# Optimization experiments

Hardware: AMD Instinct MI355X
Metric: run time of the kernel (lower is better)

## Reference

```python
import jax, jax.numpy as jnp
import numpy as np

B, S, D, M, E, K = 2, 2048, 1024, 1408, 8, 2  # batch, seq, n_embed, n_moe_mlp, n_experts, top_k


def setup_inputs() -> dict:
    key = jax.random.key(0)
    k0, k1, k2, k3, k4 = jax.random.split(key, 5)
    scale = 0.02
    return {
        "x": jax.random.normal(k0, (B, S, D), dtype=jnp.float32),
        "w_gate": jax.random.normal(k1, (D, E), dtype=jnp.float32) * scale,  # gate.weight.T
        "w_g": jax.random.normal(k2, (E, D, M), dtype=jnp.float32) * scale,  # gate_proj.weight.T per expert
        "w_u": jax.random.normal(k3, (E, D, M), dtype=jnp.float32) * scale,  # up_proj.weight.T per expert
        "w_d": jax.random.normal(k4, (E, M, D), dtype=jnp.float32) * scale,  # down_proj.weight.T per expert
    }


def reference(x, w_gate, w_g, w_u, w_d):
    # router
    scores = x @ w_gate                                  # [B,S,E]
    topk_scores, topk_idx = jax.lax.top_k(scores, K)     # [B,S,K]
    topk_probs = jax.nn.softmax(topk_scores, axis=-1)    # softmax over selected experts only
    # scatter top-k probs back to dense [B,S,E] gating (top_k indices are distinct)
    gating = jnp.sum(
        jax.nn.one_hot(topk_idx, E, dtype=topk_probs.dtype) * topk_probs[..., None],
        axis=-2,
    )                                                    # [B,S,E]
    # dense all-expert SwiGLU (faithful to the compute-then-mask original)
    hidden = jax.nn.silu(jnp.einsum("bsd,edm->ebsm", x, w_g)) * jnp.einsum(
        "bsd,edm->ebsm", x, w_u
    )                                                    # [E,B,S,M]
    expert_out = jnp.einsum("ebsm,emd->ebsd", hidden, w_d)  # [E,B,S,D]
    # masked weighted combine
    y = jnp.einsum("bse,ebsd->bsd", gating, expert_out)  # [B,S,D]
    return y
```

## Files before the change

kernel.cpp:

```cpp
#include <hip/hip_runtime.h>
#include <cstdio>

constexpr int T  = 4096;
constexpr int D  = 1024;
constexpr int M  = 1408;
constexpr int E  = 8;

constexpr int TM = 128;
constexpr int TN = 128;
constexpr int BK = 32;
constexpr int RCAP = T * 2 + E * TM;
constexpr int MT_MAX = T / TM;
constexpr int NT_UP = M / TN;
constexpr int NT_DN = D / TN;

constexpr int CSTR = 64;
constexpr int TOKB = 64;

typedef _Float16 half8 __attribute__((ext_vector_type(8)));
typedef _Float16 half4 __attribute__((ext_vector_type(4)));
typedef float    floatx4 __attribute__((ext_vector_type(4)));

constexpr size_t OFF_COUNTS = 0;
constexpr size_t OFF_BASE   = (size_t)E * CSTR * 4;
constexpr size_t OFF_PC     = OFF_BASE + 64;
constexpr size_t OFF_TOTAL  = OFF_PC + 64;
constexpr size_t OFF_T2E    = OFF_TOTAL + 64;
constexpr size_t OFF_T2POS  = OFF_T2E   + (size_t)2 * T * 4;
constexpr size_t OFF_T2P    = OFF_T2POS + (size_t)2 * T * 4;
constexpr size_t OFF_TLIST  = OFF_T2P   + (size_t)2 * T * 4;
constexpr size_t OFF_XG     = OFF_TLIST + (size_t)E * T * 4;
constexpr size_t OFF_HID    = OFF_XG  + (size_t)RCAP * D * 2;
constexpr size_t OFF_WGT    = OFF_HID + (size_t)RCAP * M * 2;
constexpr size_t OFF_WUT    = OFF_WGT + (size_t)E * M * D * 2;
constexpr size_t OFF_WDT    = OFF_WUT + (size_t)E * M * D * 2;
constexpr size_t WS_NEED    = OFF_WDT + (size_t)E * D * M * 2;

__device__ __forceinline__ void gl_lds16(const void* g, void* l) {
  __builtin_amdgcn_global_load_lds(
      (const __attribute__((address_space(1))) unsigned int*)g,
      (__attribute__((address_space(3))) unsigned int*)l, 16, 0, 0);
}

__global__ __launch_bounds__(256) void k_router(
    const float* __restrict__ x, const float* __restrict__ wgate,
    int* __restrict__ counts, int* __restrict__ tlist,
    int* __restrict__ t2e, int* __restrict__ t2pos, float* __restrict__ t2p) {
  __shared__ int   s_cnt[E];
  __shared__ int   s_base[E];
  __shared__ int   s_e[2 * TOKB];
  __shared__ int   s_pos[2 * TOKB];
  __shared__ float s_p[2 * TOKB];
  int wv = threadIdx.x >> 6, lane = threadIdx.x & 63;
  if (threadIdx.x < E) s_cnt[threadIdx.x] = 0;
  __syncthreads();

  for (int j = 0; j < TOKB / 4; ++j) {
    int tl = wv * (TOKB / 4) + j;
    int t  = blockIdx.x * TOKB + tl;
    const float* xr = x + (size_t)t * D;
    float acc[E] = {0.f,0.f,0.f,0.f,0.f,0.f,0.f,0.f};
    #pragma unroll
    for (int i = 0; i < D / 64; ++i) {
      int d = i * 64 + lane;
      float xv = xr[d];
      const float4* wr2 = (const float4*)(wgate + (size_t)d * E);
      float4 w0 = wr2[0], w1 = wr2[1];
      acc[0] += xv * w0.x; acc[1] += xv * w0.y; acc[2] += xv * w0.z; acc[3] += xv * w0.w;
      acc[4] += xv * w1.x; acc[5] += xv * w1.y; acc[6] += xv * w1.z; acc[7] += xv * w1.w;
    }
    #pragma unroll
    for (int e = 0; e < E; ++e) {
      #pragma unroll
      for (int off = 32; off; off >>= 1) acc[e] += __shfl_xor(acc[e], off, 64);
    }
    if (lane == 0) {
      int i0 = 0; float s0 = acc[0];
      #pragma unroll
      for (int e = 1; e < E; ++e) if (acc[e] > s0) { s0 = acc[e]; i0 = e; }
      int i1 = -1; float s1 = -1e30f;
      #pragma unroll
      for (int e = 0; e < E; ++e) if (e != i0 && acc[e] > s1) { s1 = acc[e]; i1 = e; }
      float p0 = 1.f / (1.f + expf(s1 - s0));
      float p1 = 1.f - p0;
      int q0 = atomicAdd(&s_cnt[i0], 1);
      int q1 = atomicAdd(&s_cnt[i1], 1);
      s_e[2 * tl]     = i0; s_pos[2 * tl]     = q0; s_p[2 * tl]     = p0;
      s_e[2 * tl + 1] = i1; s_pos[2 * tl + 1] = q1; s_p[2 * tl + 1] = p1;
    }
  }
  __syncthreads();
  if (threadIdx.x < E)
    s_base[threadIdx.x] = atomicAdd(&counts[threadIdx.x * CSTR], s_cnt[threadIdx.x]);
  __syncthreads();
  if (threadIdx.x < 2 * TOKB) {
    int sl = threadIdx.x;
    int e = s_e[sl];
    int pos = s_base[e] + s_pos[sl];
    int t = blockIdx.x * TOKB + (sl >> 1);
    tlist[e * T + pos] = t;
    t2e[2 * t + (sl & 1)]   = e;
    t2pos[2 * t + (sl & 1)] = pos;
    t2p[2 * t + (sl & 1)]   = s_p[sl];
  }
}

__global__ void k_scan(const int* __restrict__ counts, int* __restrict__ base,
                       int* __restrict__ pc, int* __restrict__ total) {
  if (threadIdx.x == 0 && blockIdx.x == 0) {
    int b = 0;
    for (int e = 0; e < E; ++e) {
      base[e] = b;
      int p = (counts[e * CSTR] + TM - 1) / TM * TM;
      pc[e] = p; b += p;
    }
    *total = b;
  }
}

__global__ __launch_bounds__(256) void k_gather(
    const float* __restrict__ x, const int* __restrict__ counts,
    const int* __restrict__ base, const int* __restrict__ pc,
    const int* __restrict__ total, const int* __restrict__ tlist,
    _Float16* __restrict__ Xg) {
  int r = blockIdx.x;
  if (r >= *total) return;
  int e = 0;
  while (e < E - 1 && r >= base[e] + pc[e]) ++e;
  int local = r - base[e];
  int d = threadIdx.x * 4;
  union { _Float16 h[4]; ushort4 u; } o;
  if (local < counts[e * CSTR]) {
    int t = tlist[e * T + local];
    float4 v = *(const float4*)(x + (size_t)t * D + d);
    o.h[0] = (_Float16)v.x; o.h[1] = (_Float16)v.y;
    o.h[2] = (_Float16)v.z; o.h[3] = (_Float16)v.w;
  } else {
    o.h[0] = (_Float16)0.f; o.h[1] = (_Float16)0.f;
    o.h[2] = (_Float16)0.f; o.h[3] = (_Float16)0.f;
  }
  *(ushort4*)(Xg + (size_t)r * D + d) = o.u;
}

__global__ __launch_bounds__(256) void k_transpose(
    const float* __restrict__ src, _Float16* __restrict__ dst, int R, int C) {
  __shared__ float tile[32][33];
  int e = blockIdx.z, rt = blockIdx.y, ct = blockIdx.x;
  int tr  = threadIdx.x >> 3;
  int tc4 = (threadIdx.x & 7) * 4;
  const float* s = src + ((size_t)e * R + rt * 32 + tr) * C + ct * 32 + tc4;
  float4 v = *(const float4*)s;
  tile[tr][tc4 + 0] = v.x; tile[tr][tc4 + 1] = v.y;
  tile[tr][tc4 + 2] = v.z; tile[tr][tc4 + 3] = v.w;
  __syncthreads();
  union { _Float16 h[4]; ushort4 u; } o;
  #pragma unroll
  for (int i = 0; i < 4; ++i) o.h[i] = (_Float16)tile[tc4 + i][tr];
  *(ushort4*)(dst + ((size_t)e * C + ct * 32 + tr) * R + rt * 32 + tc4) = o.u;
}

__global__ __launch_bounds__(256, 2) void k_upgate(
    const _Float16* __restrict__ Xg, const _Float16* __restrict__ wgT,
    const _Float16* __restrict__ wuT, _Float16* __restrict__ Hid,
    const int* __restrict__ base, const int* __restrict__ pc) {
  int lin = blockIdx.x;
  int e = lin & 7;
  int r = lin >> 3;
  int nt = r % NT_UP;
  int mt = r / NT_UP;
  if (mt * TM >= pc[e]) return;
  int row0 = base[e] + mt * TM;
  int n0 = nt * TN;
  __shared__ _Float16 As[TM * BK];
  __shared__ _Float16 Bg[TN * BK];
  __shared__ _Float16 Bu[TN * BK];
  int tid = threadIdx.x;
  int w = tid >> 6, lane = tid & 63;
  int lrow = lane & 15, quad = lane >> 4;
  int wr = w >> 1, wc = w & 1;
  int sr = lane >> 2, sc = (lane & 3) * 8;

  const _Float16* wg_e = wgT + (size_t)e * M * D;
  const _Float16* wu_e = wuT + (size_t)e * M * D;
  const _Float16* pA0 = Xg + (size_t)(row0 + w * 32 + sr) * D + sc;
  const _Float16* pA1 = Xg + (size_t)(row0 + w * 32 + 16 + sr) * D + sc;
  const _Float16* pG0 = wg_e + (size_t)(n0 + w * 32 + sr) * D + sc;
  const _Float16* pG1 = wg_e + (size_t)(n0 + w * 32 + 16 + sr) * D + sc;
  const _Float16* pU0 = wu_e + (size_t)(n0 + w * 32 + sr) * D + sc;
  const _Float16* pU1 = wu_e + (size_t)(n0 + w * 32 + 16 + sr) * D + sc;
  char* lA0 = (char*)As + (w * 2 + 0) * 1024;
  char* lA1 = (char*)As + (w * 2 + 1) * 1024;
  char* lG0 = (char*)Bg + (w * 2 + 0) * 1024;
  char* lG1 = (char*)Bg + (w * 2 + 1) * 1024;
  char* lU0 = (char*)Bu + (w * 2 + 0) * 1024;
  char* lU1 = (char*)Bu + (w * 2 + 1) * 1024;

  floatx4 accg[4][4] = {};
  floatx4 accu[4][4] = {};

  for (int k0 = 0; k0 < D; k0 += BK) {
    gl_lds16(pA0, lA0); gl_lds16(pA1, lA1);
    gl_lds16(pG0, lG0); gl_lds16(pG1, lG1);
    gl_lds16(pU0, lU0); gl_lds16(pU1, lU1);
    pA0 += BK; pA1 += BK; pG0 += BK; pG1 += BK; pU0 += BK; pU1 += BK;
    __syncthreads();
    half8 af[4];
    #pragma unroll
    for (int i = 0; i < 4; ++i)
      af[i] = *(const half8*)&As[(wr * 64 + i * 16 + lrow) * BK + quad * 8];
    #pragma unroll
    for (int c = 0; c < 4; ++c) {
      half8 bgc = *(const half8*)&Bg[(wc * 64 + c * 16 + lrow) * BK + quad * 8];
      half8 buc = *(const half8*)&Bu[(wc * 64 + c * 16 + lrow) * BK + quad * 8];
      #pragma unroll
      for (int i = 0; i < 4; ++i) {
        accg[c][i] = __builtin_amdgcn_mfma_f32_16x16x32_f16(af[i], bgc, accg[c][i], 0, 0, 0);
        accu[c][i] = __builtin_amdgcn_mfma_f32_16x16x32_f16(af[i], buc, accu[c][i], 0, 0, 0);
      }
    }
    __syncthreads();
  }
  #pragma unroll
  for (int c = 0; c < 4; ++c) {
    int col = n0 + wc * 64 + c * 16 + lrow;
    #pragma unroll
    for (int i = 0; i < 4; ++i) {
      int rowb = row0 + wr * 64 + i * 16 + quad * 4;
      #pragma unroll
      for (int reg = 0; reg < 4; ++reg) {
        float g = accg[c][i][reg], u = accu[c][i][reg];
        Hid[(size_t)(rowb + reg) * M + col] = (_Float16)(g / (1.f + expf(-g)) * u);
      }
    }
  }
}

__global__ __launch_bounds__(256, 2) void k_down(
    const _Float16* __restrict__ Hid, const _Float16* __restrict__ wdT,
    _Float16* __restrict__ Yp,
    const int* __restrict__ base, const int* __restrict__ pc) {
  int lin = blockIdx.x;
  int e = lin & 7;
  int r = lin >> 3;
  int nt = r % NT_DN;
  int mt = r / NT_DN;
  if (mt * TM >= pc[e]) return;
  int row0 = base[e] + mt * TM;
  int d0 = nt * TN;
  __shared__ _Float16 As[TM * BK];
  __shared__ _Float16 Bs[TN * BK];
  int tid = threadIdx.x;
  int w = tid >> 6, lane = tid & 63;
  int lrow = lane & 15, quad = lane >> 4;
  int wr = w >> 1, wc = w & 1;
  int sr = lane >> 2, sc = (lane & 3) * 8;

  const _Float16* wd_e = wdT + (size_t)e * D * M;
  const _Float16* pA0 = Hid + (size_t)(row0 + w * 32 + sr) * M + sc;
  const _Float16* pA1 = Hid + (size_t)(row0 + w * 32 + 16 + sr) * M + sc;
  const _Float16* pB0 = wd_e + (size_t)(d0 + w * 32 + sr) * M + sc;
  const _Float16* pB1 = wd_e + (size_t)(d0 + w * 32 + 16 + sr) * M + sc;
  char* lA0 = (char*)As + (w * 2 + 0) * 1024;
  char* lA1 = (char*)As + (w * 2 + 1) * 1024;
  char* lB0 = (char*)Bs + (w * 2 + 0) * 1024;
  char* lB1 = (char*)Bs + (w * 2 + 1) * 1024;

  floatx4 acc[4][4] = {};

  for (int k0 = 0; k0 < M; k0 += BK) {
    gl_lds16(pA0, lA0); gl_lds16(pA1, lA1);
    gl_lds16(pB0, lB0); gl_lds16(pB1, lB1);
    pA0 += BK; pA1 += BK; pB0 += BK; pB1 += BK;
    __syncthreads();
    half8 af[4];
    #pragma unroll
    for (int i = 0; i < 4; ++i)
      af[i] = *(const half8*)&As[(wr * 64 + i * 16 + lrow) * BK + quad * 8];
    #pragma unroll
    for (int c = 0; c < 4; ++c) {
      half8 bc = *(const half8*)&Bs[(wc * 64 + c * 16 + lrow) * BK + quad * 8];
      #pragma unroll
      for (int i = 0; i < 4; ++i)
        acc[c][i] = __builtin_amdgcn_mfma_f32_16x16x32_f16(af[i], bc, acc[c][i], 0, 0, 0);
    }
    __syncthreads();
  }
  #pragma unroll
  for (int c = 0; c < 4; ++c) {
    int col = d0 + wc * 64 + c * 16 + lrow;
    #pragma unroll
    for (int i = 0; i < 4; ++i) {
      int rowb = row0 + wr * 64 + i * 16 + quad * 4;
      #pragma unroll
      for (int reg = 0; reg < 4; ++reg)
        Yp[(size_t)(rowb + reg) * D + col] = (_Float16)acc[c][i][reg];
    }
  }
}

__global__ __launch_bounds__(256) void k_combine(
    const _Float16* __restrict__ Yp, const int* __restrict__ base,
    const int* __restrict__ t2e, const int* __restrict__ t2pos,
    const float* __restrict__ t2p, float* __restrict__ out) {
  int t = blockIdx.x;
  int r0 = base[t2e[2 * t]]     + t2pos[2 * t];
  int r1 = base[t2e[2 * t + 1]] + t2pos[2 * t + 1];
  float p0 = t2p[2 * t], p1 = t2p[2 * t + 1];
  int d = threadIdx.x * 4;
  half4 h0 = *(const half4*)(Yp + (size_t)r0 * D + d);
  half4 h1 = *(const half4*)(Yp + (size_t)r1 * D + d);
  float4 o;
  o.x = p0 * (float)h0.x + p1 * (float)h1.x;
  o.y = p0 * (float)h0.y + p1 * (float)h1.y;
  o.z = p0 * (float)h0.z + p1 * (float)h1.z;
  o.w = p0 * (float)h0.w + p1 * (float)h1.w;
  *(float4*)(out + (size_t)t * D + d) = o;
}

extern "C" void kernel_launch(void* const* d_in, const int* in_sizes, int n_in,
                              void* d_out, int out_size, void* d_ws, size_t ws_size,
                              hipStream_t stream) {
  const float* x     = (const float*)d_in[0];
  const float* wgate = (const float*)d_in[1];
  const float* w_g   = (const float*)d_in[2];
  const float* w_u   = (const float*)d_in[3];
  const float* w_d   = (const float*)d_in[4];
  float* out = (float*)d_out;
  char* ws = (char*)d_ws;

  if (ws_size < WS_NEED) {
    fprintf(stderr, "kernel_launch: ws_size=%zu < needed %zu\n", ws_size, WS_NEED);
    return;
  }

  int* counts = (int*)(ws + OFF_COUNTS);
  int* base   = (int*)(ws + OFF_BASE);
  int* pcn    = (int*)(ws + OFF_PC);
  int* total  = (int*)(ws + OFF_TOTAL);
  int* t2e    = (int*)(ws + OFF_T2E);
  int* t2pos  = (int*)(ws + OFF_T2POS);
  float* t2p  = (float*)(ws + OFF_T2P);
  int* tlist  = (int*)(ws + OFF_TLIST);
  _Float16* Xg  = (_Float16*)(ws + OFF_XG);
  _Float16* Hid = (_Float16*)(ws + OFF_HID);
  _Float16* wgT = (_Float16*)(ws + OFF_WGT);
  _Float16* wuT = (_Float16*)(ws + OFF_WUT);
  _Float16* wdT = (_Float16*)(ws + OFF_WDT);

  hipMemsetAsync(ws, 0, OFF_T2E, stream);

  k_router<<<T / TOKB, 256, 0, stream>>>(x, wgate, counts, tlist, t2e, t2pos, t2p);
  k_scan<<<1, 64, 0, stream>>>(counts, base, pcn, total);
  k_gather<<<RCAP, 256, 0, stream>>>(x, counts, base, pcn, total, tlist, Xg);

  k_transpose<<<dim3(M / 32, D / 32, E), 256, 0, stream>>>(w_g, wgT, D, M);
  k_transpose<<<dim3(M / 32, D / 32, E), 256, 0, stream>>>(w_u, wuT, D, M);
  k_transpose<<<dim3(D / 32, M / 32, E), 256, 0, stream>>>(w_d, wdT, M, D);

  k_upgate<<<E * MT_MAX * NT_UP, 256, 0, stream>>>(Xg, wgT, wuT, Hid, base, pcn);
  _Float16* Yp = Xg;
  k_down<<<E * MT_MAX * NT_DN, 256, 0, stream>>>(Hid, wdT, Yp, base, pcn);
  k_combine<<<T, 256, 0, stream>>>(Yp, base, t2e, t2pos, t2p, out);
}
```

Baseline: 348.6 us.

## Fuse router and weight transposes into one prep kernel, drop scan, double BK

Merges the router and the three weight transpose/cast kernels into a single k_prep launch, and shrinks the router token block so more blocks run. Removes the serial scan kernel by having each consumer recompute expert base offsets from the counts. Doubles the GEMM K-tile to 64 so each LDS stage feeds twice as many MFMAs per barrier, which doubles shared memory per block and may lower occupancy.

```diff
diff --git a/kernel.cpp b/kernel.cpp
--- a/kernel.cpp
+++ b/kernel.cpp
@@ -8,14 +8,17 @@
 
 constexpr int TM = 128;
 constexpr int TN = 128;
-constexpr int BK = 32;
+constexpr int BK = 64;
 constexpr int RCAP = T * 2 + E * TM;
 constexpr int MT_MAX = T / TM;
 constexpr int NT_UP = M / TN;
 constexpr int NT_DN = D / TN;
 
 constexpr int CSTR = 64;
-constexpr int TOKB = 64;
+constexpr int TOKB = 16;
+constexpr int RTB  = T / TOKB;
+constexpr int TP_PER_W = (M / 32) * (D / 32) * E;
+constexpr int PREP_GRID = RTB + 3 * TP_PER_W;
 
 typedef _Float16 half8 __attribute__((ext_vector_type(8)));
 typedef _Float16 half4 __attribute__((ext_vector_type(4)));
@@ -42,95 +45,128 @@
       (__attribute__((address_space(3))) unsigned int*)l, 16, 0, 0);
 }
 
-__global__ __launch_bounds__(256) void k_router(
+__device__ __forceinline__ void expert_base_pc(const int* __restrict__ counts,
+                                               int e, int& base_e, int& pc_e) {
+  int b = 0; base_e = 0; pc_e = 0;
+  #pragma unroll
+  for (int ee = 0; ee < E; ++ee) {
+    int c = counts[ee * CSTR];
+    int p = (c + TM - 1) / TM * TM;
+    if (ee == e) { base_e = b; pc_e = p; }
+    b += p;
+  }
+}
+
+__global__ __launch_bounds__(256) void k_prep(
     const float* __restrict__ x, const float* __restrict__ wgate,
+    const float* __restrict__ w_g, const float* __restrict__ w_u,
+    const float* __restrict__ w_d,
+    _Float16* __restrict__ wgT, _Float16* __restrict__ wuT, _Float16* __restrict__ wdT,
     int* __restrict__ counts, int* __restrict__ tlist,
     int* __restrict__ t2e, int* __restrict__ t2pos, float* __restrict__ t2p) {
+  __shared__ float tile[32][33];
   __shared__ int   s_cnt[E];
   __shared__ int   s_base[E];
   __shared__ int   s_e[2 * TOKB];
   __shared__ int   s_pos[2 * TOKB];
   __shared__ float s_p[2 * TOKB];
-  int wv = threadIdx.x >> 6, lane = threadIdx.x & 63;
-  if (threadIdx.x < E) s_cnt[threadIdx.x] = 0;
+  int bid = blockIdx.x;
+
+  if (bid < RTB) {
+    int wv = threadIdx.x >> 6, lane = threadIdx.x & 63;
+    if (threadIdx.x < E) s_cnt[threadIdx.x] = 0;
+    __syncthreads();
+    for (int j = 0; j < TOKB / 4; ++j) {
+      int tl = wv * (TOKB / 4) + j;
+      int t  = bid * TOKB + tl;
+      const float* xr = x + (size_t)t * D;
+      float acc[E] = {0.f,0.f,0.f,0.f,0.f,0.f,0.f,0.f};
+      #pragma unroll
+      for (int i = 0; i < D / 64; ++i) {
+        int d = i * 64 + lane;
+        float xv = xr[d];
+        const float4* wr2 = (const float4*)(wgate + (size_t)d * E);
+        float4 w0 = wr2[0], w1 = wr2[1];
+        acc[0] += xv * w0.x; acc[1] += xv * w0.y; acc[2] += xv * w0.z; acc[3] += xv * w0.w;
+        acc[4] += xv * w1.x; acc[5] += xv * w1.y; acc[6] += xv * w1.z; acc[7] += xv * w1.w;
+      }
+      #pragma unroll
+      for (int e = 0; e < E; ++e) {
+        #pragma unroll
+        for (int off = 32; off; off >>= 1) acc[e] += __shfl_xor(acc[e], off, 64);
+      }
+      if (lane == 0) {
+        int i0 = 0; float s0 = acc[0];
+        #pragma unroll
+        for (int e = 1; e < E; ++e) if (acc[e] > s0) { s0 = acc[e]; i0 = e; }
+        int i1 = -1; float s1 = -1e30f;
+        #pragma unroll
+        for (int e = 0; e < E; ++e) if (e != i0 && acc[e] > s1) { s1 = acc[e]; i1 = e; }
+        float p0 = 1.f / (1.f + expf(s1 - s0));
+        float p1 = 1.f - p0;
+        int q0 = atomicAdd(&s_cnt[i0], 1);
+        int q1 = atomicAdd(&s_cnt[i1], 1);
+        s_e[2 * tl]     = i0; s_pos[2 * tl]     = q0; s_p[2 * tl]     = p0;
+        s_e[2 * tl + 1] = i1; s_pos[2 * tl + 1] = q1; s_p[2 * tl + 1] = p1;
+      }
+    }
+    __syncthreads();
+    if (threadIdx.x < E)
+      s_base[threadIdx.x] = atomicAdd(&counts[threadIdx.x * CSTR], s_cnt[threadIdx.x]);
+    __syncthreads();
+    if (threadIdx.x < 2 * TOKB) {
+      int sl = threadIdx.x;
+      int e = s_e[sl];
+      int pos = s_base[e] + s_pos[sl];
+      int t = bid * TOKB + (sl >> 1);
+      tlist[e * T + pos] = t;
+      t2e[2 * t + (sl & 1)]   = e;
+      t2pos[2 * t + (sl & 1)] = pos;
+      t2p[2 * t + (sl & 1)]   = s_p[sl];
+    }
+    return;
+  }
+
+  int i = bid - RTB;
+  int which = i / TP_PER_W;
+  int j = i - which * TP_PER_W;
+  const float* src; _Float16* dst; int Rr, Cc;
+  if (which == 0)      { src = w_g; dst = wgT; Rr = D; Cc = M; }
+  else if (which == 1) { src = w_u; dst = wuT; Rr = D; Cc = M; }
+  else                 { src = w_d; dst = wdT; Rr = M; Cc = D; }
+  int ctn = Cc / 32, rtn = Rr / 32;
+  int e   = j / (ctn * rtn);
+  int rem = j - e * (ctn * rtn);
+  int rt = rem / ctn, ct = rem - rt * ctn;
+  int tr  = threadIdx.x >> 3;
+  int tc4 = (threadIdx.x & 7) * 4;
+  const float* s = src + ((size_t)e * Rr + rt * 32 + tr) * Cc + ct * 32 + tc4;
+  float4 v = *(const float4*)s;
+  tile[tr][tc4 + 0] = v.x; tile[tr][tc4 + 1] = v.y;
+  tile[tr][tc4 + 2] = v.z; tile[tr][tc4 + 3] = v.w;
   __syncthreads();
-
-  for (int j = 0; j < TOKB / 4; ++j) {
-    int tl = wv * (TOKB / 4) + j;
-    int t  = blockIdx.x * TOKB + tl;
-    const float* xr = x + (size_t)t * D;
-    float acc[E] = {0.f,0.f,0.f,0.f,0.f,0.f,0.f,0.f};
-    #pragma unroll
-    for (int i = 0; i < D / 64; ++i) {
-      int d = i * 64 + lane;
-      float xv = xr[d];
-      const float4* wr2 = (const float4*)(wgate + (size_t)d * E);
-      float4 w0 = wr2[0], w1 = wr2[1];
-      acc[0] += xv * w0.x; acc[1] += xv * w0.y; acc[2] += xv * w0.z; acc[3] += xv * w0.w;
-      acc[4] += xv * w1.x; acc[5] += xv * w1.y; acc[6] += xv * w1.z; acc[7] += xv * w1.w;
-    }
-    #pragma unroll
-    for (int e = 0; e < E; ++e) {
-      #pragma unroll
-      for (int off = 32; off; off >>= 1) acc[e] += __shfl_xor(acc[e], off, 64);
-    }
-    if (lane == 0) {
-      int i0 = 0; float s0 = acc[0];
-      #pragma unroll
-      for (int e = 1; e < E; ++e) if (acc[e] > s0) { s0 = acc[e]; i0 = e; }
-      int i1 = -1; float s1 = -1e30f;
-      #pragma unroll
-      for (int e = 0; e < E; ++e) if (e != i0 && acc[e] > s1) { s1 = acc[e]; i1 = e; }
-      float p0 = 1.f / (1.f + expf(s1 - s0));
-      float p1 = 1.f - p0;
-      int q0 = atomicAdd(&s_cnt[i0], 1);
-      int q1 = atomicAdd(&s_cnt[i1], 1);
-      s_e[2 * tl]     = i0; s_pos[2 * tl]     = q0; s_p[2 * tl]     = p0;
-      s_e[2 * tl + 1] = i1; s_pos[2 * tl + 1] = q1; s_p[2 * tl + 1] = p1;
-    }
-  }
-  __syncthreads();
-  if (threadIdx.x < E)
-    s_base[threadIdx.x] = atomicAdd(&counts[threadIdx.x * CSTR], s_cnt[threadIdx.x]);
-  __syncthreads();
-  if (threadIdx.x < 2 * TOKB) {
-    int sl = threadIdx.x;
-    int e = s_e[sl];
-    int pos = s_base[e] + s_pos[sl];
-    int t = blockIdx.x * TOKB + (sl >> 1);
-    tlist[e * T + pos] = t;
-    t2e[2 * t + (sl & 1)]   = e;
-    t2pos[2 * t + (sl & 1)] = pos;
-    t2p[2 * t + (sl & 1)]   = s_p[sl];
-  }
-}
-
-__global__ void k_scan(const int* __restrict__ counts, int* __restrict__ base,
-                       int* __restrict__ pc, int* __restrict__ total) {
-  if (threadIdx.x == 0 && blockIdx.x == 0) {
-    int b = 0;
-    for (int e = 0; e < E; ++e) {
-      base[e] = b;
-      int p = (counts[e * CSTR] + TM - 1) / TM * TM;
-      pc[e] = p; b += p;
-    }
-    *total = b;
-  }
+  union { _Float16 h[4]; ushort4 u; } o;
+  #pragma unroll
+  for (int q = 0; q < 4; ++q) o.h[q] = (_Float16)tile[tc4 + q][tr];
+  *(ushort4*)(dst + ((size_t)e * Cc + ct * 32 + tr) * Rr + rt * 32 + tc4) = o.u;
 }
 
 __global__ __launch_bounds__(256) void k_gather(
     const float* __restrict__ x, const int* __restrict__ counts,
-    const int* __restrict__ base, const int* __restrict__ pc,
-    const int* __restrict__ total, const int* __restrict__ tlist,
-    _Float16* __restrict__ Xg) {
+    const int* __restrict__ tlist, _Float16* __restrict__ Xg) {
   int r = blockIdx.x;
-  if (r >= *total) return;
-  int e = 0;
-  while (e < E - 1 && r >= base[e] + pc[e]) ++e;
-  int local = r - base[e];
+  int b = 0, e = -1, local = 0, cnt = 0;
+  #pragma unroll
+  for (int ee = 0; ee < E; ++ee) {
+    int c = counts[ee * CSTR];
+    int p = (c + TM - 1) / TM * TM;
+    if (e < 0 && r < b + p) { e = ee; local = r - b; cnt = c; }
+    b += p;
+  }
+  if (e < 0) return;
   int d = threadIdx.x * 4;
   union { _Float16 h[4]; ushort4 u; } o;
-  if (local < counts[e * CSTR]) {
+  if (local < cnt) {
     int t = tlist[e * T + local];
     float4 v = *(const float4*)(x + (size_t)t * D + d);
     o.h[0] = (_Float16)v.x; o.h[1] = (_Float16)v.y;
@@ -142,34 +178,19 @@
   *(ushort4*)(Xg + (size_t)r * D + d) = o.u;
 }
 
-__global__ __launch_bounds__(256) void k_transpose(
-    const float* __restrict__ src, _Float16* __restrict__ dst, int R, int C) {
-  __shared__ float tile[32][33];
-  int e = blockIdx.z, rt = blockIdx.y, ct = blockIdx.x;
-  int tr  = threadIdx.x >> 3;
-  int tc4 = (threadIdx.x & 7) * 4;
-  const float* s = src + ((size_t)e * R + rt * 32 + tr) * C + ct * 32 + tc4;
-  float4 v = *(const float4*)s;
-  tile[tr][tc4 + 0] = v.x; tile[tr][tc4 + 1] = v.y;
-  tile[tr][tc4 + 2] = v.z; tile[tr][tc4 + 3] = v.w;
-  __syncthreads();
-  union { _Float16 h[4]; ushort4 u; } o;
-  #pragma unroll
-  for (int i = 0; i < 4; ++i) o.h[i] = (_Float16)tile[tc4 + i][tr];
-  *(ushort4*)(dst + ((size_t)e * C + ct * 32 + tr) * R + rt * 32 + tc4) = o.u;
-}
-
 __global__ __launch_bounds__(256, 2) void k_upgate(
     const _Float16* __restrict__ Xg, const _Float16* __restrict__ wgT,
     const _Float16* __restrict__ wuT, _Float16* __restrict__ Hid,
-    const int* __restrict__ base, const int* __restrict__ pc) {
+    const int* __restrict__ counts) {
   int lin = blockIdx.x;
   int e = lin & 7;
   int r = lin >> 3;
   int nt = r % NT_UP;
   int mt = r / NT_UP;
-  if (mt * TM >= pc[e]) return;
-  int row0 = base[e] + mt * TM;
+  int base_e, pc_e;
+  expert_base_pc(counts, e, base_e, pc_e);
+  if (mt * TM >= pc_e) return;
+  int row0 = base_e + mt * TM;
   int n0 = nt * TN;
   __shared__ _Float16 As[TM * BK];
   __shared__ _Float16 Bg[TN * BK];
@@ -178,44 +199,50 @@
   int w = tid >> 6, lane = tid & 63;
   int lrow = lane & 15, quad = lane >> 4;
   int wr = w >> 1, wc = w & 1;
-  int sr = lane >> 2, sc = (lane & 3) * 8;
+  int sr = lane >> 3, sc = (lane & 7) * 8;
 
   const _Float16* wg_e = wgT + (size_t)e * M * D;
   const _Float16* wu_e = wuT + (size_t)e * M * D;
-  const _Float16* pA0 = Xg + (size_t)(row0 + w * 32 + sr) * D + sc;
-  const _Float16* pA1 = Xg + (size_t)(row0 + w * 32 + 16 + sr) * D + sc;
-  const _Float16* pG0 = wg_e + (size_t)(n0 + w * 32 + sr) * D + sc;
-  const _Float16* pG1 = wg_e + (size_t)(n0 + w * 32 + 16 + sr) * D + sc;
-  const _Float16* pU0 = wu_e + (size_t)(n0 + w * 32 + sr) * D + sc;
-  const _Float16* pU1 = wu_e + (size_t)(n0 + w * 32 + 16 + sr) * D + sc;
-  char* lA0 = (char*)As + (w * 2 + 0) * 1024;
-  char* lA1 = (char*)As + (w * 2 + 1) * 1024;
-  char* lG0 = (char*)Bg + (w * 2 + 0) * 1024;
-  char* lG1 = (char*)Bg + (w * 2 + 1) * 1024;
-  char* lU0 = (char*)Bu + (w * 2 + 0) * 1024;
-  char* lU1 = (char*)Bu + (w * 2 + 1) * 1024;
+  const _Float16* pA[4]; const _Float16* pG[4]; const _Float16* pU[4];
+  char* lA[4]; char* lG[4]; char* lU[4];
+  #pragma unroll
+  for (int rr = 0; rr < 4; ++rr) {
+    int grow = w * 32 + rr * 8 + sr;
+    pA[rr] = Xg   + (size_t)(row0 + grow) * D + sc;
+    pG[rr] = wg_e + (size_t)(n0   + grow) * D + sc;
+    pU[rr] = wu_e + (size_t)(n0   + grow) * D + sc;
+    lA[rr] = (char*)As + (w * 4 + rr) * 1024;
+    lG[rr] = (char*)Bg + (w * 4 + rr) * 1024;
+    lU[rr] = (char*)Bu + (w * 4 + rr) * 1024;
+  }
 
   floatx4 accg[4][4] = {};
   floatx4 accu[4][4] = {};
 
   for (int k0 = 0; k0 < D; k0 += BK) {
-    gl_lds16(pA0, lA0); gl_lds16(pA1, lA1);
-    gl_lds16(pG0, lG0); gl_lds16(pG1, lG1);
-    gl_lds16(pU0, lU0); gl_lds16(pU1, lU1);
-    pA0 += BK; pA1 += BK; pG0 += BK; pG1 += BK; pU0 += BK; pU1 += BK;
-    __syncthreads();
-    half8 af[4];
-    #pragma unroll
-    for (int i = 0; i < 4; ++i)
-      af[i] = *(const half8*)&As[(wr * 64 + i * 16 + lrow) * BK + quad * 8];
-    #pragma unroll
-    for (int c = 0; c < 4; ++c) {
-      half8 bgc = *(const half8*)&Bg[(wc * 64 + c * 16 + lrow) * BK + quad * 8];
-      half8 buc = *(const half8*)&Bu[(wc * 64 + c * 16 + lrow) * BK + quad * 8];
-      #pragma unroll
-      for (int i = 0; i < 4; ++i) {
-        accg[c][i] = __builtin_amdgcn_mfma_f32_16x16x32_f16(af[i], bgc, accg[c][i], 0, 0, 0);
-        accu[c][i] = __builtin_amdgcn_mfma_f32_16x16x32_f16(af[i], buc, accu[c][i], 0, 0, 0);
+    #pragma unroll
+    for (int rr = 0; rr < 4; ++rr) {
+      gl_lds16(pA[rr], lA[rr]);
+      gl_lds16(pG[rr], lG[rr]);
+      gl_lds16(pU[rr], lU[rr]);
+      pA[rr] += BK; pG[rr] += BK; pU[rr] += BK;
+    }
+    __syncthreads();
+    #pragma unroll
+    for (int c2 = 0; c2 < 2; ++c2) {
+      half8 af[4];
+      #pragma unroll
+      for (int i = 0; i < 4; ++i)
+        af[i] = *(const half8*)&As[(wr * 64 + i * 16 + lrow) * BK + c2 * 32 + quad * 8];
+      #pragma unroll
+      for (int c = 0; c < 4; ++c) {
+        half8 bgc = *(const half8*)&Bg[(wc * 64 + c * 16 + lrow) * BK + c2 * 32 + quad * 8];
+        half8 buc = *(const half8*)&Bu[(wc * 64 + c * 16 + lrow) * BK + c2 * 32 + quad * 8];
+        #pragma unroll
+        for (int i = 0; i < 4; ++i) {
+          accg[c][i] = __builtin_amdgcn_mfma_f32_16x16x32_f16(af[i], bgc, accg[c][i], 0, 0, 0);
+          accu[c][i] = __builtin_amdgcn_mfma_f32_16x16x32_f16(af[i], buc, accu[c][i], 0, 0, 0);
+        }
       }
     }
     __syncthreads();
@@ -237,15 +264,16 @@
 
 __global__ __launch_bounds__(256, 2) void k_down(
     const _Float16* __restrict__ Hid, const _Float16* __restrict__ wdT,
-    _Float16* __restrict__ Yp,
-    const int* __restrict__ base, const int* __restrict__ pc) {
+    _Float16* __restrict__ Yp, const int* __restrict__ counts) {
   int lin = blockIdx.x;
   int e = lin & 7;
   int r = lin >> 3;
   int nt = r % NT_DN;
   int mt = r / NT_DN;
-  if (mt * TM >= pc[e]) return;
-  int row0 = base[e] + mt * TM;
+  int base_e, pc_e;
+  expert_base_pc(counts, e, base_e, pc_e);
+  if (mt * TM >= pc_e) return;
+  int row0 = base_e + mt * TM;
   int d0 = nt * TN;
   __shared__ _Float16 As[TM * BK];
   __shared__ _Float16 Bs[TN * BK];
@@ -253,35 +281,43 @@
   int w = tid >> 6, lane = tid & 63;
   int lrow = lane & 15, quad = lane >> 4;
   int wr = w >> 1, wc = w & 1;
-  int sr = lane >> 2, sc = (lane & 3) * 8;
+  int sr = lane >> 3, sc = (lane & 7) * 8;
 
   const _Float16* wd_e = wdT + (size_t)e * D * M;
-  const _Float16* pA0 = Hid + (size_t)(row0 + w * 32 + sr) * M + sc;
-  const _Float16* pA1 = Hid + (size_t)(row0 + w * 32 + 16 + sr) * M + sc;
-  const _Float16* pB0 = wd_e + (size_t)(d0 + w * 32 + sr) * M + sc;
-  const _Float16* pB1 = wd_e + (size_t)(d0 + w * 32 + 16 + sr) * M + sc;
-  char* lA0 = (char*)As + (w * 2 + 0) * 1024;
-  char* lA1 = (char*)As + (w * 2 + 1) * 1024;
-  char* lB0 = (char*)Bs + (w * 2 + 0) * 1024;
-  char* lB1 = (char*)Bs + (w * 2 + 1) * 1024;
+  const _Float16* pA[4]; const _Float16* pB[4];
+  char* lA[4]; char* lB[4];
+  #pragma unroll
+  for (int rr = 0; rr < 4; ++rr) {
+    int grow = w * 32 + rr * 8 + sr;
+    pA[rr] = Hid  + (size_t)(row0 + grow) * M + sc;
+    pB[rr] = wd_e + (size_t)(d0   + grow) * M + sc;
+    lA[rr] = (char*)As + (w * 4 + rr) * 1024;
+    lB[rr] = (char*)Bs + (w * 4 + rr) * 1024;
+  }
 
   floatx4 acc[4][4] = {};
 
   for (int k0 = 0; k0 < M; k0 += BK) {
-    gl_lds16(pA0, lA0); gl_lds16(pA1, lA1);
-    gl_lds16(pB0, lB0); gl_lds16(pB1, lB1);
-    pA0 += BK; pA1 += BK; pB0 += BK; pB1 += BK;
-    __syncthreads();
-    half8 af[4];
-    #pragma unroll
-    for (int i = 0; i < 4; ++i)
-      af[i] = *(const half8*)&As[(wr * 64 + i * 16 + lrow) * BK + quad * 8];
-    #pragma unroll
-    for (int c = 0; c < 4; ++c) {
-      half8 bc = *(const half8*)&Bs[(wc * 64 + c * 16 + lrow) * BK + quad * 8];
+    #pragma unroll
+    for (int rr = 0; rr < 4; ++rr) {
+      gl_lds16(pA[rr], lA[rr]);
+      gl_lds16(pB[rr], lB[rr]);
+      pA[rr] += BK; pB[rr] += BK;
+    }
+    __syncthreads();
+    #pragma unroll
+    for (int c2 = 0; c2 < 2; ++c2) {
+      half8 af[4];
       #pragma unroll
       for (int i = 0; i < 4; ++i)
-        acc[c][i] = __builtin_amdgcn_mfma_f32_16x16x32_f16(af[i], bc, acc[c][i], 0, 0, 0);
+        af[i] = *(const half8*)&As[(wr * 64 + i * 16 + lrow) * BK + c2 * 32 + quad * 8];
+      #pragma unroll
+      for (int c = 0; c < 4; ++c) {
+        half8 bc = *(const half8*)&Bs[(wc * 64 + c * 16 + lrow) * BK + c2 * 32 + quad * 8];
+        #pragma unroll
+        for (int i = 0; i < 4; ++i)
+          acc[c][i] = __builtin_amdgcn_mfma_f32_16x16x32_f16(af[i], bc, acc[c][i], 0, 0, 0);
+      }
     }
     __syncthreads();
   }
@@ -299,12 +335,21 @@
 }
 
 __global__ __launch_bounds__(256) void k_combine(
-    const _Float16* __restrict__ Yp, const int* __restrict__ base,
+    const _Float16* __restrict__ Yp, const int* __restrict__ counts,
     const int* __restrict__ t2e, const int* __restrict__ t2pos,
     const float* __restrict__ t2p, float* __restrict__ out) {
   int t = blockIdx.x;
-  int r0 = base[t2e[2 * t]]     + t2pos[2 * t];
-  int r1 = base[t2e[2 * t + 1]] + t2pos[2 * t + 1];
+  int e0 = t2e[2 * t], e1 = t2e[2 * t + 1];
+  int b = 0, b0 = 0, b1 = 0;
+  #pragma unroll
+  for (int ee = 0; ee < E; ++ee) {
+    if (ee == e0) b0 = b;
+    if (ee == e1) b1 = b;
+    int c = counts[ee * CSTR];
+    b += (c + TM - 1) / TM * TM;
+  }
+  int r0 = b0 + t2pos[2 * t];
+  int r1 = b1 + t2pos[2 * t + 1];
   float p0 = t2p[2 * t], p1 = t2p[2 * t + 1];
   int d = threadIdx.x * 4;
   half4 h0 = *(const half4*)(Yp + (size_t)r0 * D + d);
@@ -334,9 +379,6 @@
   }
 
   int* counts = (int*)(ws + OFF_COUNTS);
-  int* base   = (int*)(ws + OFF_BASE);
-  int* pcn    = (int*)(ws + OFF_PC);
-  int* total  = (int*)(ws + OFF_TOTAL);
   int* t2e    = (int*)(ws + OFF_T2E);
   int* t2pos  = (int*)(ws + OFF_T2POS);
   float* t2p  = (float*)(ws + OFF_T2P);
@@ -347,18 +389,14 @@
   _Float16* wuT = (_Float16*)(ws + OFF_WUT);
   _Float16* wdT = (_Float16*)(ws + OFF_WDT);
 
-  hipMemsetAsync(ws, 0, OFF_T2E, stream);
-
-  k_router<<<T / TOKB, 256, 0, stream>>>(x, wgate, counts, tlist, t2e, t2pos, t2p);
-  k_scan<<<1, 64, 0, stream>>>(counts, base, pcn, total);
-  k_gather<<<RCAP, 256, 0, stream>>>(x, counts, base, pcn, total, tlist, Xg);
-
-  k_transpose<<<dim3(M / 32, D / 32, E), 256, 0, stream>>>(w_g, wgT, D, M);
-  k_transpose<<<dim3(M / 32, D / 32, E), 256, 0, stream>>>(w_u, wuT, D, M);
-  k_transpose<<<dim3(D / 32, M / 32, E), 256, 0, stream>>>(w_d, wdT, M, D);
-
-  k_upgate<<<E * MT_MAX * NT_UP, 256, 0, stream>>>(Xg, wgT, wuT, Hid, base, pcn);
+  hipMemsetAsync(counts, 0, (size_t)E * CSTR * 4, stream);
+
+  k_prep<<<PREP_GRID, 256, 0, stream>>>(x, wgate, w_g, w_u, w_d,
+                                        wgT, wuT, wdT,
+                                        counts, tlist, t2e, t2pos, t2p);
+  k_gather<<<RCAP, 256, 0, stream>>>(x, counts, tlist, Xg);
+  k_upgate<<<E * MT_MAX * NT_UP, 256, 0, stream>>>(Xg, wgT, wuT, Hid, counts);
   _Float16* Yp = Xg;
-  k_down<<<E * MT_MAX * NT_DN, 256, 0, stream>>>(Hid, wdT, Yp, base, pcn);
-  k_combine<<<T, 256, 0, stream>>>(Yp, base, t2e, t2pos, t2p, out);
-}
+  k_down<<<E * MT_MAX * NT_DN, 256, 0, stream>>>(Hid, wdT, Yp, counts);
+  k_combine<<<T, 256, 0, stream>>>(Yp, counts, t2e, t2pos, t2p, out);
+}
```

After: 339.1 us. 2.7% less time.
